# Kernel optimization log

Measured on AMD Instinct MI355X. Metric: run time of the kernel, lower is better.

Reference implementation:

```python
import jax, jax.numpy as jnp
import numpy as np

B, E, S, H = 4, 1024, 1024, 16
HD = E // H  # head_size = 64
MASK_VALUE = -1000000000.0
W_SCALE = 0.05  # keep pre-softmax logits moderate since original softmax is not max-stabilized


def setup_inputs() -> dict:
    key = jax.random.key(0)
    ks = jax.random.split(key, 7)
    queries = jax.random.normal(ks[0], (B, E, S), jnp.float32)
    keys = jax.random.normal(ks[1], (B, E, S), jnp.float32)
    values = jax.random.normal(ks[2], (B, E, S), jnp.float32)
    # causal multiplicative mask, broadcast over batch
    mask = jnp.broadcast_to(jnp.tril(jnp.ones((S, S), jnp.float32)), (B, S, S))
    Wq = jax.random.normal(ks[3], (H, HD, HD), jnp.float32) * W_SCALE
    Wk = jax.random.normal(ks[4], (H, HD, HD), jnp.float32) * W_SCALE
    Wv = jax.random.normal(ks[5], (H, HD, HD), jnp.float32) * W_SCALE
    Wf = jax.random.normal(ks[6], (E, E), jnp.float32) * W_SCALE
    return dict(queries=queries, keys=keys, values=values, mask=mask,
                Wq=Wq, Wk=Wk, Wv=Wv, Wf=Wf)


def reference(queries, keys, values, mask, Wq, Wk, Wv, Wf):
    # channels-first: [B, E, S] -> split embedding axis into heads: [B, H, HD, S]
    qh = queries.reshape(B, H, HD, S)
    kh = keys.reshape(B, H, HD, S)
    vh = values.reshape(B, H, HD, S)
    # per-head linear projections: W[h] @ x_slice, batched over heads
    q = jnp.einsum('hde,bhes->bhds', Wq, qh)
    k = jnp.einsum('hde,bhes->bhds', Wk, kh)
    v = jnp.einsum('hde,bhes->bhds', Wv, vh)
    # pre_softmax = Q^T @ K / sqrt(head_size)  -> [B, H, S, S]
    pre = jnp.einsum('bhds,bhdt->bhst', q, k) / jnp.sqrt(jnp.float32(HD))
    m = mask[:, None, :, :]  # broadcast mask over heads
    pre = pre * m + (m == 0).astype(jnp.float32) * MASK_VALUE
    # Faithful to original: exp / reduce_sum(axis=-1)[..., None, :]
    # i.e. post[b,h,i,j] = exp(pre[b,h,i,j]) / sum_t exp(pre[b,h,j,t])
    e = jnp.exp(pre)
    post = e / jnp.sum(e, axis=3)[:, :, None, :]
    # values @ post^T : out[b,h,d,i] = sum_j v[b,h,d,j] * post[b,h,i,j]
    out_h = jnp.einsum('bhdj,bhij->bhdi', v, post)
    pre_linear = out_h.reshape(B, E, S)  # concat heads along embedding axis
    return jnp.einsum('ef,bfs->bes', Wf, pre_linear)
```

## Files before the change

kernel.cpp:

```cpp
#include <hip/hip_runtime.h>
#include <hip/hip_bf16.h>
#include <stdint.h>

#define NB 4
#define NH 16
#define HDIM 64
#define NS 1024
#define NE 1024

typedef __bf16 bf16x8 __attribute__((ext_vector_type(8)));
typedef __bf16 bf16x2_t __attribute__((ext_vector_type(2)));
typedef float f32x4 __attribute__((ext_vector_type(4)));
typedef float f32x16 __attribute__((ext_vector_type(16)));
typedef unsigned int uint4v __attribute__((ext_vector_type(4)));
typedef unsigned int uint2v __attribute__((ext_vector_type(2)));
typedef unsigned short u16;

#if defined(__has_builtin)
#if __has_builtin(__builtin_amdgcn_global_load_lds)
#define HAVE_GLDS 1
#endif
#endif

__device__ __forceinline__ u16 f2bf(float f) {
  return __builtin_bit_cast(u16, (__bf16)f);
}
__device__ __forceinline__ unsigned pk2(float a, float b) {
  bf16x2_t v; v[0] = (__bf16)a; v[1] = (__bf16)b;
  return __builtin_bit_cast(unsigned, v);
}
__device__ __forceinline__ float fexp2(float x) {
#if defined(__has_builtin)
#if __has_builtin(__builtin_amdgcn_exp2f)
  return __builtin_amdgcn_exp2f(x);
#else
  return __expf(x * 0.69314718056f);
#endif
#else
  return __expf(x * 0.69314718056f);
#endif
}
__device__ __forceinline__ f32x4 mfma16(bf16x8 a, bf16x8 b, f32x4 c) {
  return __builtin_amdgcn_mfma_f32_16x16x32_bf16(a, b, c, 0, 0, 0);
}
__device__ __forceinline__ f32x16 mfma32(bf16x8 a, bf16x8 b, f32x16 c) {
  return __builtin_amdgcn_mfma_f32_32x32x16_bf16(a, b, c, 0, 0, 0);
}
__device__ __forceinline__ bf16x8 ld_bf8(const u16* p) {
  return __builtin_bit_cast(bf16x8, *(const uint4v*)p);
}
#ifdef HAVE_GLDS
__device__ __forceinline__ void gld16(const void* g, void* l) {
  __builtin_amdgcn_global_load_lds(
      (__attribute__((address_space(1))) void*)g,
      (__attribute__((address_space(3))) void*)l, 16, 0, 0);
}
#endif

#if defined(__has_builtin)
#if __has_builtin(__builtin_amdgcn_permlane32_swap)
#define HAVE_PLS 1
#endif
#endif
__device__ __forceinline__ uint2v plswap(unsigned a, unsigned b) {
#ifdef HAVE_PLS
  return __builtin_amdgcn_permlane32_swap(a, b, false, false);
#else
  unsigned asw = (unsigned)__shfl_xor((int)a, 32);
  unsigned bsw = (unsigned)__shfl_xor((int)b, 32);
  bool hi = (threadIdx.x & 32) != 0;
  uint2v r;
  r[0] = hi ? bsw : a;
  r[1] = hi ? b : asw;
  return r;
#endif
}

__global__ __launch_bounds__(256) void proj_kernel(
    const float* __restrict__ q_in, const float* __restrict__ k_in,
    const float* __restrict__ v_in, const float* __restrict__ Wq,
    const float* __restrict__ Wk, const float* __restrict__ Wv,
    const float* __restrict__ Wf,
    u16* __restrict__ qT, u16* __restrict__ kT, u16* __restrict__ vv,
    u16* __restrict__ Wf16)
{
  const int which = blockIdx.z;
  const int tid = threadIdx.x;

  if (which == 3) {
    int chunk = blockIdx.y * 4 + blockIdx.x;
    #pragma unroll
    for (int jj = 0; jj < 4; ++jj) {
      int i = chunk * 1024 + tid + 256 * jj;
      float4 f = ((const float4*)Wf)[i];
      uint2v p;
      p[0] = pk2(f.x, f.y);
      p[1] = pk2(f.z, f.w);
      ((uint2v*)Wf16)[i] = p;
    }
    return;
  }

  const int bh = blockIdx.y;
  const int b = bh >> 4, h = bh & 15;
  const int s0 = blockIdx.x * 256;
  const int w = tid >> 6, l = tid & 63, lr = l & 15, lg = l >> 4;

  const float* x = (which == 0) ? q_in : (which == 1) ? k_in : v_in;
  const float* W = ((which == 0) ? Wq : (which == 1) ? Wk : Wv) + h * 4096;
  const float wsc = (which == 0) ? 0.18033688f : 1.0f;

  __shared__ alignas(16) u16 xT[256][72];
  __shared__ alignas(16) u16 Wl[64][72];

  #pragma unroll
  for (int j = 0; j < 4; ++j) {
    int i = tid * 4 + j;
    int d = i >> 4;
    int e0 = (i & 15) * 4;
    float4 f = *(const float4*)(W + d * 64 + e0);
    uint2v p;
    p[0] = pk2(f.x * wsc, f.y * wsc);
    p[1] = pk2(f.z * wsc, f.w * wsc);
    *(uint2v*)&Wl[d][e0] = p;
  }
  {
    const float* xp = x + ((size_t)b * NE + h * 64) * NS + s0 + tid;
    #pragma unroll
    for (int j = 0; j < 8; ++j) {
      uint4v pk;
      #pragma unroll
      for (int q = 0; q < 4; ++q) {
        float f0 = xp[(size_t)(j * 8 + q * 2) * NS];
        float f1 = xp[(size_t)(j * 8 + q * 2 + 1) * NS];
        pk[q] = pk2(f0, f1);
      }
      *(uint4v*)&xT[tid][j * 8] = pk;
    }
  }
  __syncthreads();

  bf16x8 af[4][2];
  #pragma unroll
  for (int mt = 0; mt < 4; ++mt) {
    af[mt][0] = ld_bf8(&Wl[mt * 16 + lr][lg * 8]);
    af[mt][1] = ld_bf8(&Wl[mt * 16 + lr][32 + lg * 8]);
  }
  f32x4 acc[4][4] = {};
  #pragma unroll
  for (int nt = 0; nt < 4; ++nt) {
    bf16x8 b0 = ld_bf8(&xT[w * 64 + nt * 16 + lr][lg * 8]);
    bf16x8 b1 = ld_bf8(&xT[w * 64 + nt * 16 + lr][32 + lg * 8]);
    #pragma unroll
    for (int mt = 0; mt < 4; ++mt) {
      acc[mt][nt] = mfma16(af[mt][0], b0, acc[mt][nt]);
      acc[mt][nt] = mfma16(af[mt][1], b1, acc[mt][nt]);
    }
  }

  if (which < 2) {
    u16* o = ((which == 0) ? qT : kT) + (size_t)bh * NS * 64;
    #pragma unroll
    for (int mt = 0; mt < 4; ++mt)
      #pragma unroll
      for (int nt = 0; nt < 4; ++nt) {
        int s = s0 + w * 64 + nt * 16 + lr;
        int d = mt * 16 + lg * 4;
        uint2v p;
        p[0] = pk2(acc[mt][nt][0], acc[mt][nt][1]);
        p[1] = pk2(acc[mt][nt][2], acc[mt][nt][3]);
        *(uint2v*)(o + (size_t)s * 64 + d) = p;
      }
  } else {
    u16* o = vv + (size_t)bh * 64 * NS;
    #pragma unroll
    for (int mt = 0; mt < 4; ++mt)
      #pragma unroll
      for (int nt = 0; nt < 4; ++nt)
        #pragma unroll
        for (int jr = 0; jr < 4; ++jr) {
          int d = mt * 16 + lg * 4 + jr;
          int s = s0 + w * 64 + nt * 16 + lr;
          o[(size_t)d * NS + s] = f2bf(acc[mt][nt][jr]);
        }
  }
}

__global__ __launch_bounds__(512) void denom_kernel(
    const u16* __restrict__ qT, const u16* __restrict__ kT,
    float* __restrict__ l2rDg)
{
  const int wg = blockIdx.x;
  const int rt = 7 - (wg >> 6);
  const int bh = wg & 63;
  const int i0 = rt * 128;
  const int tid = threadIdx.x, w = tid >> 6, l = tid & 63, lr = l & 15, lg = l >> 4;
  __shared__ alignas(16) u16 klds[128][72];
  const u16* qb = qT + (size_t)bh * NS * 64;
  const u16* kb = kT + (size_t)bh * NS * 64;
  const int gi = i0 + w * 16 + lr;
  bf16x8 bq0 = ld_bf8(qb + (size_t)gi * 64 + lg * 8);
  bf16x8 bq1 = ld_bf8(qb + (size_t)gi * 64 + 32 + lg * 8);
  float den = 0.f;
  const int nkt = rt + 1;
  uint4v kreg[2];
  const int krow = tid >> 3, kcx = tid & 7;
  #pragma unroll
  for (int j = 0; j < 2; ++j)
    kreg[j] = *(const uint4v*)(kb + (size_t)(krow + j * 64) * 64 + kcx * 8);
  for (int t = 0; t < nkt; ++t) {
    __syncthreads();
    #pragma unroll
    for (int j = 0; j < 2; ++j)
      *(uint4v*)&klds[krow + j * 64][kcx * 8] = kreg[j];
    __syncthreads();
    const int t0 = t * 128;
    if (t + 1 < nkt) {
      #pragma unroll
      for (int j = 0; j < 2; ++j)
        kreg[j] = *(const uint4v*)(kb + (size_t)(t0 + 128 + krow + j * 64) * 64 + kcx * 8);
    }
    if (t + 1 < nkt) {
      #pragma unroll
      for (int mt = 0; mt < 8; ++mt) {
        bf16x8 a0 = ld_bf8(&klds[mt * 16 + lr][lg * 8]);
        bf16x8 a1 = ld_bf8(&klds[mt * 16 + lr][32 + lg * 8]);
        f32x4 z = {0.f, 0.f, 0.f, 0.f};
        f32x4 sc = mfma16(a0, bq0, z);
        sc = mfma16(a1, bq1, sc);
        den += fexp2(sc[0]) + fexp2(sc[1]) + fexp2(sc[2]) + fexp2(sc[3]);
      }
    } else {
      #pragma unroll
      for (int mt = 0; mt < 8; ++mt) {
        bf16x8 a0 = ld_bf8(&klds[mt * 16 + lr][lg * 8]);
        bf16x8 a1 = ld_bf8(&klds[mt * 16 + lr][32 + lg * 8]);
        f32x4 z = {0.f, 0.f, 0.f, 0.f};
        f32x4 sc = mfma16(a0, bq0, z);
        sc = mfma16(a1, bq1, sc);
        #pragma unroll
        for (int r = 0; r < 4; ++r) {
          int gt = t0 + mt * 16 + lg * 4 + r;
          den += (gt <= gi) ? fexp2(sc[r]) : 0.f;
        }
      }
    }
  }
  den += __shfl_xor(den, 16);
  den += __shfl_xor(den, 32);
  if (l < 16) l2rDg[(size_t)bh * NS + gi] = -__log2f(den);
}

__global__ __launch_bounds__(256) void attn_kernel(
    const u16* __restrict__ qT, const u16* __restrict__ kT,
    const u16* __restrict__ vv, const float* __restrict__ l2rDg,
    u16* __restrict__ X)
{
  const int wg = blockIdx.x;
  const int rt = 15 - (wg >> 6);
  const int bh = wg & 63;
  const int b = bh >> 4, h = bh & 15;
  const int i0 = rt * 64;
  const int tid = threadIdx.x, w = tid >> 6, l = tid & 63;
  const int q5 = l & 31, hf = l >> 5;
  const int qi = w >> 1, ki = w & 1;

  __shared__ alignas(16) unsigned char smem[2 * 64 * 72 * 2 * 2 + 2 * 64 * 4];
  typedef u16 (*tile_t)[64][72];
  tile_t klds = (tile_t)smem;
  tile_t vlds = (tile_t)(smem + 18432);
  float (*dlds)[64] = (float(*)[64])(smem + 36864);

  const u16* qb = qT + (size_t)bh * NS * 64;
  const u16* kb = kT + (size_t)bh * NS * 64;
  const u16* vb = vv + (size_t)bh * 64 * NS;
  const float* rb = l2rDg + (size_t)bh * NS;
  const int r0w = i0 + qi * 32;
  const int gi2 = r0w + q5;
  bf16x8 bq[4];
  #pragma unroll
  for (int dc = 0; dc < 4; ++dc)
    bq[dc] = ld_bf8(qb + (size_t)gi2 * 64 + dc * 16 + hf * 8);
  f32x16 acc[2] = {};
  const int nkt = rt + 1;
  uint4v kreg[2], vreg[2];
  float dreg = 0.f;
  const int crow = tid >> 3, ccx = tid & 7;
  #pragma unroll
  for (int j = 0; j < 2; ++j) {
    kreg[j] = *(const uint4v*)(kb + (size_t)(crow + j * 32) * 64 + ccx * 8);
    vreg[j] = *(const uint4v*)(vb + (size_t)(crow + j * 32) * NS + ccx * 8);
  }
  if (tid < 64) dreg = rb[tid];
  #pragma unroll
  for (int j = 0; j < 2; ++j) {
    *(uint4v*)&klds[0][crow + j * 32][ccx * 8] = kreg[j];
    *(uint4v*)&vlds[0][crow + j * 32][ccx * 8] = vreg[j];
  }
  if (tid < 64) dlds[0][tid] = dreg;
  __syncthreads();
  int p = 0;
  for (int t = 0; t < nkt; ++t) {
    const int t0 = t * 64;
    const bool more = (t + 1 < nkt);
    if (more) {
      const int t0n = t0 + 64;
      #pragma unroll
      for (int j = 0; j < 2; ++j) {
        kreg[j] = *(const uint4v*)(kb + (size_t)(t0n + crow + j * 32) * 64 + ccx * 8);
        vreg[j] = *(const uint4v*)(vb + (size_t)(crow + j * 32) * NS + t0n + ccx * 8);
      }
      if (tid < 64) dreg = rb[t0n + tid];
    }
    const int kb0 = t0 + ki * 32;
    if (kb0 <= r0w + 31) {
      const bool msk = (kb0 + 31 > r0w);
      f32x16 sc = {};
      #pragma unroll
      for (int dc = 0; dc < 4; ++dc) {
        bf16x8 ak = ld_bf8(&klds[p][ki * 32 + q5][dc * 16 + hf * 8]);
        sc = mfma32(ak, bq[dc], sc);
      }
      f32x4 lv[4];
      #pragma unroll
      for (int g = 0; g < 4; ++g)
        lv[g] = *(const f32x4*)&dlds[p][ki * 32 + 4 * hf + 8 * g];
      float pe[16];
      if (!msk) {
        #pragma unroll
        for (int r = 0; r < 16; ++r)
          pe[r] = fexp2(sc[r] + lv[r >> 2][r & 3]);
      } else {
        #pragma unroll
        for (int r = 0; r < 16; ++r) {
          int key = kb0 + (r & 3) + 8 * (r >> 2) + 4 * hf;
          float e = fexp2(sc[r] + lv[r >> 2][r & 3]);
          pe[r] = (key <= gi2) ? e : 0.f;
        }
      }
      bf16x8 pa[2];
      #pragma unroll
      for (int f = 0; f < 2; ++f) {
        unsigned A0 = pk2(pe[8 * f + 0], pe[8 * f + 1]);
        unsigned A1 = pk2(pe[8 * f + 2], pe[8 * f + 3]);
        unsigned B0 = pk2(pe[8 * f + 4], pe[8 * f + 5]);
        unsigned B1 = pk2(pe[8 * f + 6], pe[8 * f + 7]);
        uint2v s0 = plswap(A0, B0);
        uint2v s1 = plswap(A1, B1);
        uint4v fw;
        fw[0] = s0[0]; fw[1] = s1[0]; fw[2] = s0[1]; fw[3] = s1[1];
        pa[f] = __builtin_bit_cast(bf16x8, fw);
      }
      __builtin_amdgcn_s_setprio(1);
      #pragma unroll
      for (int db = 0; db < 2; ++db) {
        #pragma unroll
        for (int f = 0; f < 2; ++f) {
          bf16x8 bv = ld_bf8(&vlds[p][db * 32 + q5][ki * 32 + f * 16 + hf * 8]);
          acc[db] = mfma32(pa[f], bv, acc[db]);
        }
      }
      __builtin_amdgcn_s_setprio(0);
    }
    if (more) {
      #pragma unroll
      for (int j = 0; j < 2; ++j) {
        *(uint4v*)&klds[p ^ 1][crow + j * 32][ccx * 8] = kreg[j];
        *(uint4v*)&vlds[p ^ 1][crow + j * 32][ccx * 8] = vreg[j];
      }
      if (tid < 64) dlds[p ^ 1][tid] = dreg;
      __syncthreads();
      p ^= 1;
    }
  }
  __syncthreads();
  float* flds = (float*)smem;
  if (ki == 1) {
    #pragma unroll
    for (int db = 0; db < 2; ++db)
      #pragma unroll
      for (int r = 0; r < 16; ++r) {
        int qrow = (r & 3) + 8 * (r >> 2) + 4 * hf;
        flds[(qi * 32 + qrow) * 64 + db * 32 + q5] = acc[db][r];
      }
  }
  __syncthreads();
  if (ki == 0) {
    u16* Xp = X + (size_t)b * NS * NE + h * 64;
    #pragma unroll
    for (int db = 0; db < 2; ++db)
      #pragma unroll
      for (int r = 0; r < 16; ++r) {
        int qrow = (r & 3) + 8 * (r >> 2) + 4 * hf;
        float v = acc[db][r] + flds[(qi * 32 + qrow) * 64 + db * 32 + q5];
        int srow = r0w + qrow;
        Xp[(size_t)srow * NE + db * 32 + q5] = f2bf(v);
      }
  }
}

__global__ __launch_bounds__(512) void final_gemm(
    const u16* __restrict__ Wf16, const u16* __restrict__ X,
    float* __restrict__ out)
{
  const int b = blockIdx.z;
  const int e0 = blockIdx.y * 128;
  const int s0 = blockIdx.x * 128;
  const int tid = threadIdx.x, w = tid >> 6, l = tid & 63, lr = l & 15, lg = l >> 4;
  const int wm = (w >> 2) * 64, wn = (w & 3) * 32;
  __shared__ alignas(16) u16 Ald[2][128][64];
  __shared__ alignas(16) u16 Bld[2][128][64];
  const u16* Xb = X + (size_t)b * NS * NE;
  f32x4 acc[4][2] = {};

  #define FG_ISSUE(p, k0)                                                     \
    {                                                                         \
      _Pragma("unroll")                                                       \
      for (int j = 0; j < 2; ++j) {                                           \
        int c = tid + 512 * j;                                                \
        int r = c >> 3;                                                       \
        int sc_ = ((c & 7) * 16) ^ ((r & 7) << 4);                            \
        const char* ga = (const char*)(Wf16 + (size_t)(e0 + r) * NE + (k0)) + sc_; \
        const char* gb = (const char*)(Xb + (size_t)(s0 + r) * NE + (k0)) + sc_;   \
        char* la = (char*)&Ald[p][0][0] + c * 16;                             \
        char* lb = (char*)&Bld[p][0][0] + c * 16;                             \
        STAGE16(ga, la);                                                      \
        STAGE16(gb, lb);                                                      \
      }                                                                       \
    }
#ifdef HAVE_GLDS
  #define STAGE16(g, l_) gld16((g), (l_))
#else
  #define STAGE16(g, l_) (*(uint4v*)(l_) = *(const uint4v*)(g))
#endif

  FG_ISSUE(0, 0);
  __syncthreads();
  for (int t = 0; t < 16; ++t) {
    const int p = t & 1;
    if (t < 15) FG_ISSUE(p ^ 1, (t + 1) * 64);
    __builtin_amdgcn_s_setprio(1);
    #pragma unroll
    for (int kk = 0; kk < 2; ++kk) {
      bf16x8 a[4], bb[2];
      #pragma unroll
      for (int mt = 0; mt < 4; ++mt) {
        int R = wm + mt * 16 + lr;
        a[mt] = ld_bf8((const u16*)((const char*)&Ald[p][R][0] +
                                    ((kk * 64 + lg * 16) ^ ((R & 7) << 4))));
      }
      #pragma unroll
      for (int nt = 0; nt < 2; ++nt) {
        int R = wn + nt * 16 + lr;
        bb[nt] = ld_bf8((const u16*)((const char*)&Bld[p][R][0] +
                                     ((kk * 64 + lg * 16) ^ ((R & 7) << 4))));
      }
      #pragma unroll
      for (int mt = 0; mt < 4; ++mt)
        #pragma unroll
        for (int nt = 0; nt < 2; ++nt)
          acc[mt][nt] = mfma16(a[mt], bb[nt], acc[mt][nt]);
    }
    __builtin_amdgcn_s_setprio(0);
    __syncthreads();
  }
  #pragma unroll
  for (int mt = 0; mt < 4; ++mt)
    #pragma unroll
    for (int nt = 0; nt < 2; ++nt) {
      int e = e0 + wm + mt * 16 + lg * 4;
      int s = s0 + wn + nt * 16 + lr;
      float* op = out + ((size_t)b * NE + e) * NS + s;
      op[0] = acc[mt][nt][0];
      op[NS] = acc[mt][nt][1];
      op[2 * NS] = acc[mt][nt][2];
      op[3 * NS] = acc[mt][nt][3];
    }
}

extern "C" void kernel_launch(void* const* d_in, const int* in_sizes, int n_in,
                              void* d_out, int out_size, void* d_ws, size_t ws_size,
                              hipStream_t stream) {
  (void)in_sizes; (void)n_in; (void)out_size; (void)ws_size;
  const float* q_in = (const float*)d_in[0];
  const float* k_in = (const float*)d_in[1];
  const float* v_in = (const float*)d_in[2];
  const float* Wq = (const float*)d_in[4];
  const float* Wk = (const float*)d_in[5];
  const float* Wv = (const float*)d_in[6];
  const float* Wf = (const float*)d_in[7];

  u16* qT = (u16*)d_ws;
  u16* kT = qT + (size_t)NB * NH * NS * HDIM;
  u16* vv = kT + (size_t)NB * NH * NS * HDIM;
  u16* X  = vv + (size_t)NB * NH * HDIM * NS;
  u16* Wf16 = X + (size_t)NB * NS * NE;
  float* l2rD = (float*)(Wf16 + (size_t)NE * NE);

  proj_kernel<<<dim3(4, 64, 4), 256, 0, stream>>>(q_in, k_in, v_in, Wq, Wk, Wv,
                                                  Wf, qT, kT, vv, Wf16);
  denom_kernel<<<dim3(512), 512, 0, stream>>>(qT, kT, l2rD);
  attn_kernel<<<dim3(1024), 256, 0, stream>>>(qT, kT, vv, l2rD, X);
  final_gemm<<<dim3(8, 8, 4), 512, 0, stream>>>(Wf16, X, (float*)d_out);
}
```

Baseline: 70.77 us.

## Enlarge attention tile to 128 query rows per 512-thread workgroup

The attention kernel now gives each workgroup 128 query rows and 8 waves instead of 64 rows and 4 waves. Each staged K/V tile in LDS is therefore shared by twice as many waves, which halves global K/V traffic and the number of loads per thread. The QK^T MFMA chain is also split into two independent accumulators to shorten the dependency chain. In exchange the grid is half as large, and causal load imbalance gets coarser: waves working on earlier rows sit idle through more tiles.

New measurement: 71.07 us. No clear change (+0.4%).

```diff
diff --git a/kernel.cpp b/kernel.cpp
--- a/kernel.cpp
+++ b/kernel.cpp
@@ -251,16 +251,16 @@
   if (l < 16) l2rDg[(size_t)bh * NS + gi] = -__log2f(den);
 }
 
-__global__ __launch_bounds__(256) void attn_kernel(
+__global__ __launch_bounds__(512) void attn_kernel(
     const u16* __restrict__ qT, const u16* __restrict__ kT,
     const u16* __restrict__ vv, const float* __restrict__ l2rDg,
     u16* __restrict__ X)
 {
   const int wg = blockIdx.x;
-  const int rt = 15 - (wg >> 6);
+  const int rt = 7 - (wg >> 6);
   const int bh = wg & 63;
   const int b = bh >> 4, h = bh & 15;
-  const int i0 = rt * 64;
+  const int i0 = rt * 128;
   const int tid = threadIdx.x, w = tid >> 6, l = tid & 63;
   const int q5 = l & 31, hf = l >> 5;
   const int qi = w >> 1, ki = w & 1;
@@ -282,21 +282,15 @@
   for (int dc = 0; dc < 4; ++dc)
     bq[dc] = ld_bf8(qb + (size_t)gi2 * 64 + dc * 16 + hf * 8);
   f32x16 acc[2] = {};
-  const int nkt = rt + 1;
-  uint4v kreg[2], vreg[2];
+  const int nkt = 2 * rt + 2;
+  uint4v kreg, vreg;
   float dreg = 0.f;
   const int crow = tid >> 3, ccx = tid & 7;
-  #pragma unroll
-  for (int j = 0; j < 2; ++j) {
-    kreg[j] = *(const uint4v*)(kb + (size_t)(crow + j * 32) * 64 + ccx * 8);
-    vreg[j] = *(const uint4v*)(vb + (size_t)(crow + j * 32) * NS + ccx * 8);
-  }
+  kreg = *(const uint4v*)(kb + (size_t)crow * 64 + ccx * 8);
+  vreg = *(const uint4v*)(vb + (size_t)crow * NS + ccx * 8);
   if (tid < 64) dreg = rb[tid];
-  #pragma unroll
-  for (int j = 0; j < 2; ++j) {
-    *(uint4v*)&klds[0][crow + j * 32][ccx * 8] = kreg[j];
-    *(uint4v*)&vlds[0][crow + j * 32][ccx * 8] = vreg[j];
-  }
+  *(uint4v*)&klds[0][crow][ccx * 8] = kreg;
+  *(uint4v*)&vlds[0][crow][ccx * 8] = vreg;
   if (tid < 64) dlds[0][tid] = dreg;
   __syncthreads();
   int p = 0;
@@ -305,22 +299,22 @@
     const bool more = (t + 1 < nkt);
     if (more) {
       const int t0n = t0 + 64;
-      #pragma unroll
-      for (int j = 0; j < 2; ++j) {
-        kreg[j] = *(const uint4v*)(kb + (size_t)(t0n + crow + j * 32) * 64 + ccx * 8);
-        vreg[j] = *(const uint4v*)(vb + (size_t)(crow + j * 32) * NS + t0n + ccx * 8);
-      }
+      kreg = *(const uint4v*)(kb + (size_t)(t0n + crow) * 64 + ccx * 8);
+      vreg = *(const uint4v*)(vb + (size_t)crow * NS + t0n + ccx * 8);
       if (tid < 64) dreg = rb[t0n + tid];
     }
     const int kb0 = t0 + ki * 32;
     if (kb0 <= r0w + 31) {
       const bool msk = (kb0 + 31 > r0w);
-      f32x16 sc = {};
-      #pragma unroll
-      for (int dc = 0; dc < 4; ++dc) {
-        bf16x8 ak = ld_bf8(&klds[p][ki * 32 + q5][dc * 16 + hf * 8]);
-        sc = mfma32(ak, bq[dc], sc);
-      }
+      bf16x8 ak0 = ld_bf8(&klds[p][ki * 32 + q5][0 * 16 + hf * 8]);
+      bf16x8 ak1 = ld_bf8(&klds[p][ki * 32 + q5][1 * 16 + hf * 8]);
+      bf16x8 ak2 = ld_bf8(&klds[p][ki * 32 + q5][2 * 16 + hf * 8]);
+      bf16x8 ak3 = ld_bf8(&klds[p][ki * 32 + q5][3 * 16 + hf * 8]);
+      f32x16 sa = {}, sb = {};
+      sa = mfma32(ak0, bq[0], sa);
+      sb = mfma32(ak2, bq[2], sb);
+      sa = mfma32(ak1, bq[1], sa);
+      sb = mfma32(ak3, bq[3], sb);
       f32x4 lv[4];
       #pragma unroll
       for (int g = 0; g < 4; ++g)
@@ -329,12 +323,12 @@
       if (!msk) {
         #pragma unroll
         for (int r = 0; r < 16; ++r)
-          pe[r] = fexp2(sc[r] + lv[r >> 2][r & 3]);
+          pe[r] = fexp2(sa[r] + sb[r] + lv[r >> 2][r & 3]);
       } else {
         #pragma unroll
         for (int r = 0; r < 16; ++r) {
           int key = kb0 + (r & 3) + 8 * (r >> 2) + 4 * hf;
-          float e = fexp2(sc[r] + lv[r >> 2][r & 3]);
+          float e = fexp2(sa[r] + sb[r] + lv[r >> 2][r & 3]);
           pe[r] = (key <= gi2) ? e : 0.f;
         }
       }
@@ -363,11 +357,8 @@
       __builtin_amdgcn_s_setprio(0);
     }
     if (more) {
-      #pragma unroll
-      for (int j = 0; j < 2; ++j) {
-        *(uint4v*)&klds[p ^ 1][crow + j * 32][ccx * 8] = kreg[j];
-        *(uint4v*)&vlds[p ^ 1][crow + j * 32][ccx * 8] = vreg[j];
-      }
+      *(uint4v*)&klds[p ^ 1][crow][ccx * 8] = kreg;
+      *(uint4v*)&vlds[p ^ 1][crow][ccx * 8] = vreg;
       if (tid < 64) dlds[p ^ 1][tid] = dreg;
       __syncthreads();
       p ^= 1;
@@ -500,6 +491,6 @@
   proj_kernel<<<dim3(4, 64, 4), 256, 0, stream>>>(q_in, k_in, v_in, Wq, Wk, Wv,
                                                   Wf, qT, kT, vv, Wf16);
   denom_kernel<<<dim3(512), 512, 0, stream>>>(qT, kT, l2rD);
-  attn_kernel<<<dim3(1024), 256, 0, stream>>>(qT, kT, vv, l2rD, X);
+  attn_kernel<<<dim3(512), 512, 0, stream>>>(qT, kT, vv, l2rD, X);
   final_gemm<<<dim3(8, 8, 4), 512, 0, stream>>>(Wf16, X, (float*)d_out);
 }
```

## Enlarge attention tiles to 128x128 with 512-thread workgroups

Applied to the files above, without the earlier changes.

The attention kernel now processes 128 query rows per workgroup with 8 waves, and 128-key tiles per iteration, so each wave handles two 32-key sub-blocks per step. This halves the number of K/V tile iterations and barriers per query row and improves reuse of staged K/V. The cost is more LDS per block (about 71KB), fewer workgroups (512), coarser causal load balance, and higher register pressure from holding two score accumulators.

Result: slower. 73.70 us (+4.1%).

```diff
diff --git a/kernel.cpp b/kernel.cpp
--- a/kernel.cpp
+++ b/kernel.cpp
@@ -251,25 +251,26 @@
   if (l < 16) l2rDg[(size_t)bh * NS + gi] = -__log2f(den);
 }
 
-__global__ __launch_bounds__(256) void attn_kernel(
+__global__ __launch_bounds__(512) void attn_kernel(
     const u16* __restrict__ qT, const u16* __restrict__ kT,
     const u16* __restrict__ vv, const float* __restrict__ l2rDg,
     u16* __restrict__ X)
 {
   const int wg = blockIdx.x;
-  const int rt = 15 - (wg >> 6);
+  const int rt = 7 - (wg >> 6);
   const int bh = wg & 63;
   const int b = bh >> 4, h = bh & 15;
-  const int i0 = rt * 64;
+  const int i0 = rt * 128;
   const int tid = threadIdx.x, w = tid >> 6, l = tid & 63;
   const int q5 = l & 31, hf = l >> 5;
   const int qi = w >> 1, ki = w & 1;
 
-  __shared__ alignas(16) unsigned char smem[2 * 64 * 72 * 2 * 2 + 2 * 64 * 4];
-  typedef u16 (*tile_t)[64][72];
-  tile_t klds = (tile_t)smem;
-  tile_t vlds = (tile_t)(smem + 18432);
-  float (*dlds)[64] = (float(*)[64])(smem + 36864);
+  __shared__ alignas(16) unsigned char smem[72704];
+  typedef u16 (*ktile_t)[128][72];
+  typedef u16 (*vtile_t)[64][136];
+  ktile_t klds = (ktile_t)smem;
+  vtile_t vlds = (vtile_t)(smem + 36864);
+  float (*dlds)[128] = (float(*)[128])(smem + 71680);
 
   const u16* qb = qT + (size_t)bh * NS * 64;
   const u16* kb = kT + (size_t)bh * NS * 64;
@@ -285,56 +286,69 @@
   const int nkt = rt + 1;
   uint4v kreg[2], vreg[2];
   float dreg = 0.f;
-  const int crow = tid >> 3, ccx = tid & 7;
+  const int krow = tid >> 3, kcx = tid & 7;
+  const int vrow = tid >> 4, vcx = tid & 15;
   #pragma unroll
   for (int j = 0; j < 2; ++j) {
-    kreg[j] = *(const uint4v*)(kb + (size_t)(crow + j * 32) * 64 + ccx * 8);
-    vreg[j] = *(const uint4v*)(vb + (size_t)(crow + j * 32) * NS + ccx * 8);
-  }
-  if (tid < 64) dreg = rb[tid];
+    kreg[j] = *(const uint4v*)(kb + (size_t)(krow + j * 64) * 64 + kcx * 8);
+    vreg[j] = *(const uint4v*)(vb + (size_t)(vrow + j * 32) * NS + vcx * 8);
+  }
+  if (tid < 128) dreg = rb[tid];
   #pragma unroll
   for (int j = 0; j < 2; ++j) {
-    *(uint4v*)&klds[0][crow + j * 32][ccx * 8] = kreg[j];
-    *(uint4v*)&vlds[0][crow + j * 32][ccx * 8] = vreg[j];
-  }
-  if (tid < 64) dlds[0][tid] = dreg;
+    *(uint4v*)&klds[0][krow + j * 64][kcx * 8] = kreg[j];
+    *(uint4v*)&vlds[0][vrow + j * 32][vcx * 8] = vreg[j];
+  }
+  if (tid < 128) dlds[0][tid] = dreg;
   __syncthreads();
   int p = 0;
   for (int t = 0; t < nkt; ++t) {
-    const int t0 = t * 64;
+    const int t0 = t * 128;
     const bool more = (t + 1 < nkt);
     if (more) {
-      const int t0n = t0 + 64;
+      const int t0n = t0 + 128;
       #pragma unroll
       for (int j = 0; j < 2; ++j) {
-        kreg[j] = *(const uint4v*)(kb + (size_t)(t0n + crow + j * 32) * 64 + ccx * 8);
-        vreg[j] = *(const uint4v*)(vb + (size_t)(crow + j * 32) * NS + t0n + ccx * 8);
-      }
-      if (tid < 64) dreg = rb[t0n + tid];
-    }
-    const int kb0 = t0 + ki * 32;
-    if (kb0 <= r0w + 31) {
+        kreg[j] = *(const uint4v*)(kb + (size_t)(t0n + krow + j * 64) * 64 + kcx * 8);
+        vreg[j] = *(const uint4v*)(vb + (size_t)(vrow + j * 32) * NS + t0n + vcx * 8);
+      }
+      if (tid < 128) dreg = rb[t0n + tid];
+    }
+    const int kb0 = t0 + ki * 64;
+    const int kb1 = kb0 + 32;
+    const bool a0 = (kb0 <= r0w + 31);
+    const bool a1 = (kb1 <= r0w + 31);
+    f32x16 s0v = {}, s1v = {};
+    if (a0) {
+      #pragma unroll
+      for (int dc = 0; dc < 4; ++dc) {
+        bf16x8 ak = ld_bf8(&klds[p][ki * 64 + q5][dc * 16 + hf * 8]);
+        s0v = mfma32(ak, bq[dc], s0v);
+      }
+    }
+    if (a1) {
+      #pragma unroll
+      for (int dc = 0; dc < 4; ++dc) {
+        bf16x8 ak = ld_bf8(&klds[p][ki * 64 + 32 + q5][dc * 16 + hf * 8]);
+        s1v = mfma32(ak, bq[dc], s1v);
+      }
+    }
+    if (a0) {
       const bool msk = (kb0 + 31 > r0w);
-      f32x16 sc = {};
-      #pragma unroll
-      for (int dc = 0; dc < 4; ++dc) {
-        bf16x8 ak = ld_bf8(&klds[p][ki * 32 + q5][dc * 16 + hf * 8]);
-        sc = mfma32(ak, bq[dc], sc);
-      }
       f32x4 lv[4];
       #pragma unroll
       for (int g = 0; g < 4; ++g)
-        lv[g] = *(const f32x4*)&dlds[p][ki * 32 + 4 * hf + 8 * g];
+        lv[g] = *(const f32x4*)&dlds[p][ki * 64 + 4 * hf + 8 * g];
       float pe[16];
       if (!msk) {
         #pragma unroll
         for (int r = 0; r < 16; ++r)
-          pe[r] = fexp2(sc[r] + lv[r >> 2][r & 3]);
+          pe[r] = fexp2(s0v[r] + lv[r >> 2][r & 3]);
       } else {
         #pragma unroll
         for (int r = 0; r < 16; ++r) {
           int key = kb0 + (r & 3) + 8 * (r >> 2) + 4 * hf;
-          float e = fexp2(sc[r] + lv[r >> 2][r & 3]);
+          float e = fexp2(s0v[r] + lv[r >> 2][r & 3]);
           pe[r] = (key <= gi2) ? e : 0.f;
         }
       }
@@ -356,19 +370,62 @@
       for (int db = 0; db < 2; ++db) {
         #pragma unroll
         for (int f = 0; f < 2; ++f) {
-          bf16x8 bv = ld_bf8(&vlds[p][db * 32 + q5][ki * 32 + f * 16 + hf * 8]);
+          bf16x8 bv = ld_bf8(&vlds[p][db * 32 + q5][ki * 64 + f * 16 + hf * 8]);
           acc[db] = mfma32(pa[f], bv, acc[db]);
         }
       }
       __builtin_amdgcn_s_setprio(0);
     }
+    if (a1) {
+      const bool msk = (kb1 + 31 > r0w);
+      f32x4 lv[4];
+      #pragma unroll
+      for (int g = 0; g < 4; ++g)
+        lv[g] = *(const f32x4*)&dlds[p][ki * 64 + 32 + 4 * hf + 8 * g];
+      float pe[16];
+      if (!msk) {
+        #pragma unroll
+        for (int r = 0; r < 16; ++r)
+          pe[r] = fexp2(s1v[r] + lv[r >> 2][r & 3]);
+      } else {
+        #pragma unroll
+        for (int r = 0; r < 16; ++r) {
+          int key = kb1 + (r & 3) + 8 * (r >> 2) + 4 * hf;
+          float e = fexp2(s1v[r] + lv[r >> 2][r & 3]);
+          pe[r] = (key <= gi2) ? e : 0.f;
+        }
+      }
+      bf16x8 pa[2];
+      #pragma unroll
+      for (int f = 0; f < 2; ++f) {
+        unsigned A0 = pk2(pe[8 * f + 0], pe[8 * f + 1]);
+        unsigned A1 = pk2(pe[8 * f + 2], pe[8 * f + 3]);
+        unsigned B0 = pk2(pe[8 * f + 4], pe[8 * f + 5]);
+        unsigned B1 = pk2(pe[8 * f + 6], pe[8 * f + 7]);
+        uint2v s0 = plswap(A0, B0);
+        uint2v s1 = plswap(A1, B1);
+        uint4v fw;
+        fw[0] = s0[0]; fw[1] = s1[0]; fw[2] = s0[1]; fw[3] = s1[1];
+        pa[f] = __builtin_bit_cast(bf16x8, fw);
+      }
+      __builtin_amdgcn_s_setprio(1);
+      #pragma unroll
+      for (int db = 0; db < 2; ++db) {
+        #pragma unroll
+        for (int f = 0; f < 2; ++f) {
+          bf16x8 bv = ld_bf8(&vlds[p][db * 32 + q5][ki * 64 + 32 + f * 16 + hf * 8]);
+          acc[db] = mfma32(pa[f], bv, acc[db]);
+        }
+      }
+      __builtin_amdgcn_s_setprio(0);
+    }
     if (more) {
       #pragma unroll
       for (int j = 0; j < 2; ++j) {
-        *(uint4v*)&klds[p ^ 1][crow + j * 32][ccx * 8] = kreg[j];
-        *(uint4v*)&vlds[p ^ 1][crow + j * 32][ccx * 8] = vreg[j];
-      }
-      if (tid < 64) dlds[p ^ 1][tid] = dreg;
+        *(uint4v*)&klds[p ^ 1][krow + j * 64][kcx * 8] = kreg[j];
+        *(uint4v*)&vlds[p ^ 1][vrow + j * 32][vcx * 8] = vreg[j];
+      }
+      if (tid < 128) dlds[p ^ 1][tid] = dreg;
       __syncthreads();
       p ^= 1;
     }
@@ -500,6 +557,6 @@
   proj_kernel<<<dim3(4, 64, 4), 256, 0, stream>>>(q_in, k_in, v_in, Wq, Wk, Wv,
                                                   Wf, qT, kT, vv, Wf16);
   denom_kernel<<<dim3(512), 512, 0, stream>>>(qT, kT, l2rD);
-  attn_kernel<<<dim3(1024), 256, 0, stream>>>(qT, kT, vv, l2rD, X);
+  attn_kernel<<<dim3(512), 512, 0, stream>>>(qT, kT, vv, l2rD, X);
   final_gemm<<<dim3(8, 8, 4), 512, 0, stream>>>(Wf16, X, (float*)d_out);
 }
```
